# Optimization experiments

Measured on AMD Instinct MI355X. Metric: run time of the kernel, lower is better.

Reference implementation:

```python
import jax, jax.numpy as jnp
import numpy as np

N_NODES = 50000
N_EDGES = 400000
IN_DIM = 256
OUT_DIM = 64
HEADS = 2
ATTN_HIDDEN = 64
ALPHA = 0.2
TEMP = 0.55


def setup_inputs() -> dict:
    key = jax.random.key(0)
    k_x, k_src, k_dst, k_w, k_wa, k_a = jax.random.split(key, 6)
    x = jax.random.normal(k_x, (N_NODES, IN_DIM), dtype=jnp.float32)
    src = jax.random.randint(k_src, (N_EDGES,), 0, N_NODES, dtype=jnp.int32)
    dst = jnp.sort(jax.random.randint(k_dst, (N_EDGES,), 0, N_NODES, dtype=jnp.int32))
    # Glorot-uniform-like params
    def glorot(k, shape, fan_in, fan_out):
        lim = jnp.sqrt(6.0 / (fan_in + fan_out))
        return jax.random.uniform(k, shape, jnp.float32, -lim, lim)
    W = glorot(k_w, (IN_DIM, HEADS, OUT_DIM), IN_DIM, HEADS * OUT_DIM)
    W_attn = glorot(k_wa, (HEADS, 2 * OUT_DIM, ATTN_HIDDEN), 2 * OUT_DIM, ATTN_HIDDEN)
    a_vec = glorot(k_a, (HEADS, ATTN_HIDDEN), HEADS, ATTN_HIDDEN)
    return {"x": x, "W": W, "W_attn": W_attn, "a_vec": a_vec, "src": src, "dst": dst}


def reference(x, W, W_attn, a_vec, src, dst):
    N = x.shape[0]
    # node-level projection: [N, H, F]
    Wh = jnp.einsum('nd,dhf->nhf', x, W)
    # per-edge gathers
    Wh_src = Wh[src]                                   # [E, H, F]
    Wh_dst = Wh[dst]                                   # [E, H, F]
    z = jnp.concatenate([Wh_src, Wh_dst], axis=-1)     # [E, H, 2F]
    z_act = jax.nn.leaky_relu(jnp.einsum('ehf,hfc->ehc', z, W_attn), ALPHA)
    logits = jnp.einsum('ehc,hc->eh', z_act, a_vec).astype(jnp.float32) / TEMP
    # per-head segment softmax over incoming edges of each dst node
    seg_max = jax.ops.segment_max(logits, dst, num_segments=N)   # [N, H]
    ex = jnp.exp(logits - seg_max[dst])
    seg_sum = jax.ops.segment_sum(ex, dst, num_segments=N)
    alphas = (ex / (seg_sum[dst] + 1e-9)).astype(Wh_src.dtype)   # [E, H]
    # weighted scatter-sum of source messages
    out = jax.ops.segment_sum(Wh_src * alphas[..., None], dst, num_segments=N)  # [N, H, F]
    # concat=False -> mean over heads (dropout is identity at inference)
    return out.mean(axis=1)
```

## Files before the change

kernel.cpp:

```cpp
#include <hip/hip_runtime.h>
#include <hip/hip_bf16.h>
#include <math.h>

#define N_NODES 50000
#define N_EDGES 400000
#define IN_DIM 256
#define OUT_DIM 64
#define HEADS 2
#define ATTN_HIDDEN 64
#define ALPHA_SLOPE 0.2f
#define TEMP 0.55f
#define NHF 128
#define ZDIM 384

typedef __bf16 bf16x8 __attribute__((ext_vector_type(8)));
typedef float f32x4 __attribute__((ext_vector_type(4)));

__device__ __forceinline__ ushort f2bf(float f) {
    unsigned u = __float_as_uint(f);
    u = (u + 0x7fffu + ((u >> 16) & 1u)) >> 16;
    return (ushort)u;
}
__device__ __forceinline__ unsigned pack2(float a, float b) {
    return (unsigned)f2bf(a) | ((unsigned)f2bf(b) << 16);
}
__device__ __forceinline__ float bfl(unsigned u) { return __uint_as_float(u << 16); }
__device__ __forceinline__ float bfh(unsigned u) { return __uint_as_float(u & 0xffff0000u); }

__global__ __launch_bounds__(256) void k_combine(const float* __restrict__ W,
                                                 const float* __restrict__ Wa,
                                                 ushort* __restrict__ Wctf,
                                                 const int* __restrict__ dst,
                                                 int* __restrict__ seg) {
    __shared__ float col[64];
    const int b = blockIdx.x;
    const int t = threadIdx.x;
    if (b >= ZDIM) {
        int n = (b - ZDIM) * 256 + t;
        if (n > N_NODES) return;
        int lo = 0, hi = N_EDGES;
        while (lo < hi) {
            int mid = (lo + hi) >> 1;
            if (dst[mid] < n) lo = mid + 1; else hi = mid;
        }
        seg[n] = lo;
        return;
    }
    const int n = b;
    const int k = t;
    const int c = n >> 4, r16 = n & 15;
    const int kc = k >> 5, q = (k >> 3) & 3, j = k & 7;
    const size_t pos = (size_t)(((c * 8 + kc) * 64 + q * 16 + r16)) * 8 + j;

    float val;
    if (n < 128) {
        val = W[(size_t)k * NHF + n];
    } else {
        const int part = (n - 128) >> 7;
        const int idx = (n - 128) & 127;
        const int h = idx >> 6;
        const int cc = idx & 63;
        const int fb = part ? 64 : 0;
        if (t < 64) col[t] = Wa[(size_t)h * 8192 + (size_t)(fb + t) * 64 + cc];
        __syncthreads();
        const float* wr = W + (size_t)k * NHF + h * 64;
        float acc = 0.f;
#pragma unroll
        for (int f = 0; f < 64; f++) acc += wr[f] * col[f];
        val = acc;
    }
    Wctf[pos] = f2bf(val);
}

__global__ __launch_bounds__(256, 2) void k_gemm(const float* __restrict__ x,
                                                 const ushort* __restrict__ Wctf,
                                                 ushort* __restrict__ Zb) {
    __shared__ __align__(16) ushort Bs[32768];
    const int t = threadIdx.x;
    const int w = t >> 6, lane = t & 63;
    const int q = lane >> 4, r16 = lane & 15;
    const int cbase = blockIdx.x * 8;
    const int rowbase = blockIdx.y * 128 + w * 32;

    {
        const uint4* gs = (const uint4*)(Wctf + (size_t)blockIdx.x * 32768);
        uint4* ls = (uint4*)Bs;
#pragma unroll
        for (int i = 0; i < 16; i++) ls[i * 256 + t] = gs[i * 256 + t];
    }

    int rA0 = rowbase + r16;
    int rA1 = rowbase + 16 + r16;
    rA0 = rA0 < N_NODES ? rA0 : N_NODES - 1;
    rA1 = rA1 < N_NODES ? rA1 : N_NODES - 1;
    const float* xp0 = x + (size_t)rA0 * IN_DIM + q * 8;
    const float* xp1 = x + (size_t)rA1 * IN_DIM + q * 8;

    uint4 Areg[2][8];
#pragma unroll
    for (int kc = 0; kc < 8; kc++) {
        const float4 a00 = *(const float4*)(xp0 + kc * 32);
        const float4 a01 = *(const float4*)(xp0 + kc * 32 + 4);
        const float4 a10 = *(const float4*)(xp1 + kc * 32);
        const float4 a11 = *(const float4*)(xp1 + kc * 32 + 4);
        Areg[0][kc].x = pack2(a00.x, a00.y); Areg[0][kc].y = pack2(a00.z, a00.w);
        Areg[0][kc].z = pack2(a01.x, a01.y); Areg[0][kc].w = pack2(a01.z, a01.w);
        Areg[1][kc].x = pack2(a10.x, a10.y); Areg[1][kc].y = pack2(a10.z, a10.w);
        Areg[1][kc].z = pack2(a11.x, a11.y); Areg[1][kc].w = pack2(a11.z, a11.w);
    }

    f32x4 acc[2][8];
#pragma unroll
    for (int c = 0; c < 8; c++) {
        acc[0][c] = (f32x4){0.f, 0.f, 0.f, 0.f};
        acc[1][c] = (f32x4){0.f, 0.f, 0.f, 0.f};
    }

    __syncthreads();

#pragma unroll
    for (int kc = 0; kc < 8; kc++) {
        const bf16x8 af0 = *(const bf16x8*)&Areg[0][kc];
        const bf16x8 af1 = *(const bf16x8*)&Areg[1][kc];
#pragma unroll
        for (int c = 0; c < 8; c++) {
            const bf16x8 bf = *(const bf16x8*)&Bs[((c * 8 + kc) * 64 + lane) * 8];
            acc[0][c] = __builtin_amdgcn_mfma_f32_16x16x32_bf16(af0, bf, acc[0][c], 0, 0, 0);
            acc[1][c] = __builtin_amdgcn_mfma_f32_16x16x32_bf16(af1, bf, acc[1][c], 0, 0, 0);
        }
    }
#pragma unroll
    for (int mt = 0; mt < 2; mt++)
#pragma unroll
        for (int c = 0; c < 8; c++)
#pragma unroll
            for (int rr = 0; rr < 4; rr++) {
                const int row = rowbase + mt * 16 + q * 4 + rr;
                if (row < N_NODES)
                    Zb[(size_t)row * ZDIM + (cbase + c) * 16 + r16] = f2bf(acc[mt][c][rr]);
            }
}

__global__ __launch_bounds__(256) void k_fused(const ushort* __restrict__ Zb,
                                               const float* __restrict__ avec,
                                               const int* __restrict__ src,
                                               const int* __restrict__ seg,
                                               float* __restrict__ out) {
    const int lane = threadIdx.x & 63;
    const int wv = threadIdx.x >> 6;
    const int g = lane >> 4, l16 = lane & 15;
    const int n = blockIdx.x * 16 + wv * 4 + g;
    if (n >= N_NODES) return;
    const int choff = 8 * l16;

    const float4 af0 = *(const float4*)(avec + choff);
    const float4 af1 = *(const float4*)(avec + choff + 4);
    const float a[8] = {af0.x, af0.y, af0.z, af0.w, af1.x, af1.y, af1.z, af1.w};

    const uint4 udv = *(const uint4*)(Zb + (size_t)n * ZDIM + 256 + choff);
    const float ud[8] = {bfl(udv.x), bfh(udv.x), bfl(udv.y), bfh(udv.y),
                         bfl(udv.z), bfh(udv.z), bfl(udv.w), bfh(udv.w)};

    const int e0 = seg[n], e1 = seg[n + 1];
    float m = -INFINITY, l = 0.f;
    float acc[8] = {0.f, 0.f, 0.f, 0.f, 0.f, 0.f, 0.f, 0.f};

    uint4 us = make_uint4(0, 0, 0, 0), wh = us;
    if (e0 < e1) {
        const int s = src[e0];
        us = *(const uint4*)(Zb + (size_t)s * ZDIM + 128 + choff);
        wh = *(const uint4*)(Zb + (size_t)s * ZDIM + choff);
    }
    for (int e = e0; e < e1; e++) {
        const uint4 cus = us, cwh = wh;
        if (e + 1 < e1) {
            const int sn = src[e + 1];
            us = *(const uint4*)(Zb + (size_t)sn * ZDIM + 128 + choff);
            wh = *(const uint4*)(Zb + (size_t)sn * ZDIM + choff);
        }
        float p;
        {
            float v0, v1, s0, s1;
            v0 = bfl(cus.x) + ud[0]; v1 = bfh(cus.x) + ud[1];
            s0 = fmaxf(v0, ALPHA_SLOPE * v0); s1 = fmaxf(v1, ALPHA_SLOPE * v1);
            p = s0 * a[0] + s1 * a[1];
            v0 = bfl(cus.y) + ud[2]; v1 = bfh(cus.y) + ud[3];
            s0 = fmaxf(v0, ALPHA_SLOPE * v0); s1 = fmaxf(v1, ALPHA_SLOPE * v1);
            p += s0 * a[2] + s1 * a[3];
            v0 = bfl(cus.z) + ud[4]; v1 = bfh(cus.z) + ud[5];
            s0 = fmaxf(v0, ALPHA_SLOPE * v0); s1 = fmaxf(v1, ALPHA_SLOPE * v1);
            p += s0 * a[4] + s1 * a[5];
            v0 = bfl(cus.w) + ud[6]; v1 = bfh(cus.w) + ud[7];
            s0 = fmaxf(v0, ALPHA_SLOPE * v0); s1 = fmaxf(v1, ALPHA_SLOPE * v1);
            p += s0 * a[6] + s1 * a[7];
        }
        p += __shfl_xor(p, 1, 64);
        p += __shfl_xor(p, 2, 64);
        p += __shfl_xor(p, 4, 64);
        const float logit = p * (1.0f / TEMP);
        const float nm = fmaxf(m, logit);
        const float sc = __expf(m - nm);
        const float wgt = __expf(logit - nm);
        l = l * sc + wgt;
        acc[0] = acc[0] * sc + wgt * bfl(cwh.x);
        acc[1] = acc[1] * sc + wgt * bfh(cwh.x);
        acc[2] = acc[2] * sc + wgt * bfl(cwh.y);
        acc[3] = acc[3] * sc + wgt * bfh(cwh.y);
        acc[4] = acc[4] * sc + wgt * bfl(cwh.z);
        acc[5] = acc[5] * sc + wgt * bfh(cwh.z);
        acc[6] = acc[6] * sc + wgt * bfl(cwh.w);
        acc[7] = acc[7] * sc + wgt * bfh(cwh.w);
        m = nm;
    }
    const float inv = 0.5f / (l + 1e-9f);
#pragma unroll
    for (int j = 0; j < 8; j++) {
        const float v = acc[j] * inv;
        acc[j] = v + __shfl_xor(v, 8, 64);
    }
    if (l16 < 8) {
        float4 o0 = make_float4(acc[0], acc[1], acc[2], acc[3]);
        float4 o1 = make_float4(acc[4], acc[5], acc[6], acc[7]);
        float* op = out + (size_t)n * 64 + choff;
        *(float4*)op = o0;
        *(float4*)(op + 4) = o1;
    }
}

extern "C" void kernel_launch(void* const* d_in, const int* in_sizes, int n_in,
                              void* d_out, int out_size, void* d_ws, size_t ws_size,
                              hipStream_t stream) {
    const float* x    = (const float*)d_in[0];
    const float* W    = (const float*)d_in[1];
    const float* Wa   = (const float*)d_in[2];
    const float* avec = (const float*)d_in[3];
    const int*   src  = (const int*)d_in[4];
    const int*   dst  = (const int*)d_in[5];
    float* out = (float*)d_out;

    ushort* Zb   = (ushort*)d_ws;
    ushort* Wctf = Zb + 19200000;
    int*    seg  = (int*)((char*)d_ws + 38596608);

    const int seg_blocks = (N_NODES + 1 + 255) / 256;
    k_combine <<<ZDIM + seg_blocks, 256, 0, stream>>>(W, Wa, Wctf, dst, seg);
    k_gemm    <<<dim3(3, (N_NODES + 127) / 128), 256, 0, stream>>>(x, Wctf, Zb);
    k_fused   <<<(N_NODES + 15) / 16, 256, 0, stream>>>(Zb, avec, src, seg, out);
}
```

Before: 162.5 us.

## Restructure GEMM to load x once per block and loop over column tiles

The GEMM grid changes from 3 column blocks by row blocks of 128 to a single dimension of 64-row blocks. Each block now converts its x rows to bf16 once and loops over the three 128-column slices of the combined weight, reloading the weight slice into shared memory each time. Before, x was read from global memory three times, once per column block; now it is read once. The cost is three serial weight loads into LDS per block with extra barriers, smaller per-wave M tiles (16 rows instead of 32), and more blocks in total.

Measured after the change: 157.2 us. -3.3%, faster.

```diff
diff --git a/kernel.cpp b/kernel.cpp
--- a/kernel.cpp
+++ b/kernel.cpp
@@ -79,66 +79,64 @@
     const int t = threadIdx.x;
     const int w = t >> 6, lane = t & 63;
     const int q = lane >> 4, r16 = lane & 15;
-    const int cbase = blockIdx.x * 8;
-    const int rowbase = blockIdx.y * 128 + w * 32;
+    const int rowbase = blockIdx.x * 64 + w * 16;
 
     {
-        const uint4* gs = (const uint4*)(Wctf + (size_t)blockIdx.x * 32768);
+        const uint4* gs = (const uint4*)Wctf;
         uint4* ls = (uint4*)Bs;
 #pragma unroll
         for (int i = 0; i < 16; i++) ls[i * 256 + t] = gs[i * 256 + t];
     }
 
-    int rA0 = rowbase + r16;
-    int rA1 = rowbase + 16 + r16;
-    rA0 = rA0 < N_NODES ? rA0 : N_NODES - 1;
-    rA1 = rA1 < N_NODES ? rA1 : N_NODES - 1;
-    const float* xp0 = x + (size_t)rA0 * IN_DIM + q * 8;
-    const float* xp1 = x + (size_t)rA1 * IN_DIM + q * 8;
-
-    uint4 Areg[2][8];
+    int rA = rowbase + r16;
+    rA = rA < N_NODES ? rA : N_NODES - 1;
+    const float* xp = x + (size_t)rA * IN_DIM + q * 8;
+    uint4 Areg[8];
 #pragma unroll
     for (int kc = 0; kc < 8; kc++) {
-        const float4 a00 = *(const float4*)(xp0 + kc * 32);
-        const float4 a01 = *(const float4*)(xp0 + kc * 32 + 4);
-        const float4 a10 = *(const float4*)(xp1 + kc * 32);
-        const float4 a11 = *(const float4*)(xp1 + kc * 32 + 4);
-        Areg[0][kc].x = pack2(a00.x, a00.y); Areg[0][kc].y = pack2(a00.z, a00.w);
-        Areg[0][kc].z = pack2(a01.x, a01.y); Areg[0][kc].w = pack2(a01.z, a01.w);
-        Areg[1][kc].x = pack2(a10.x, a10.y); Areg[1][kc].y = pack2(a10.z, a10.w);
-        Areg[1][kc].z = pack2(a11.x, a11.y); Areg[1][kc].w = pack2(a11.z, a11.w);
-    }
-
-    f32x4 acc[2][8];
-#pragma unroll
-    for (int c = 0; c < 8; c++) {
-        acc[0][c] = (f32x4){0.f, 0.f, 0.f, 0.f};
-        acc[1][c] = (f32x4){0.f, 0.f, 0.f, 0.f};
+        const float4 a0 = *(const float4*)(xp + kc * 32);
+        const float4 a1 = *(const float4*)(xp + kc * 32 + 4);
+        Areg[kc].x = pack2(a0.x, a0.y); Areg[kc].y = pack2(a0.z, a0.w);
+        Areg[kc].z = pack2(a1.x, a1.y); Areg[kc].w = pack2(a1.z, a1.w);
     }
 
     __syncthreads();
 
-#pragma unroll
-    for (int kc = 0; kc < 8; kc++) {
-        const bf16x8 af0 = *(const bf16x8*)&Areg[0][kc];
-        const bf16x8 af1 = *(const bf16x8*)&Areg[1][kc];
-#pragma unroll
-        for (int c = 0; c < 8; c++) {
-            const bf16x8 bf = *(const bf16x8*)&Bs[((c * 8 + kc) * 64 + lane) * 8];
-            acc[0][c] = __builtin_amdgcn_mfma_f32_16x16x32_bf16(af0, bf, acc[0][c], 0, 0, 0);
-            acc[1][c] = __builtin_amdgcn_mfma_f32_16x16x32_bf16(af1, bf, acc[1][c], 0, 0, 0);
-        }
-    }
-#pragma unroll
-    for (int mt = 0; mt < 2; mt++)
+#pragma unroll 1
+    for (int s = 0; s < 3; s++) {
+        f32x4 acc[8];
+#pragma unroll
+        for (int c = 0; c < 8; c++) acc[c] = (f32x4){0.f, 0.f, 0.f, 0.f};
+
+#pragma unroll
+        for (int kc = 0; kc < 8; kc++) {
+            const bf16x8 af = *(const bf16x8*)&Areg[kc];
+#pragma unroll
+            for (int c = 0; c < 8; c++) {
+                const bf16x8 bf = *(const bf16x8*)&Bs[((c * 8 + kc) * 64 + lane) * 8];
+                acc[c] = __builtin_amdgcn_mfma_f32_16x16x32_bf16(af, bf, acc[c], 0, 0, 0);
+            }
+        }
+
+        if (s < 2) {
+            __syncthreads();
+            const uint4* gs = (const uint4*)Wctf + (size_t)(s + 1) * 4096;
+            uint4* ls = (uint4*)Bs;
+#pragma unroll
+            for (int i = 0; i < 16; i++) ls[i * 256 + t] = gs[i * 256 + t];
+        }
+
 #pragma unroll
         for (int c = 0; c < 8; c++)
 #pragma unroll
             for (int rr = 0; rr < 4; rr++) {
-                const int row = rowbase + mt * 16 + q * 4 + rr;
+                const int row = rowbase + q * 4 + rr;
                 if (row < N_NODES)
-                    Zb[(size_t)row * ZDIM + (cbase + c) * 16 + r16] = f2bf(acc[mt][c][rr]);
+                    Zb[(size_t)row * ZDIM + (s * 8 + c) * 16 + r16] = f2bf(acc[c][rr]);
             }
+
+        if (s < 2) __syncthreads();
+    }
 }
 
 __global__ __launch_bounds__(256) void k_fused(const ushort* __restrict__ Zb,
@@ -244,6 +242,6 @@
 
     const int seg_blocks = (N_NODES + 1 + 255) / 256;
     k_combine <<<ZDIM + seg_blocks, 256, 0, stream>>>(W, Wa, Wctf, dst, seg);
-    k_gemm    <<<dim3(3, (N_NODES + 127) / 128), 256, 0, stream>>>(x, Wctf, Zb);
+    k_gemm    <<<(N_NODES + 63) / 64, 256, 0, stream>>>(x, Wctf, Zb);
     k_fused   <<<(N_NODES + 15) / 16, 256, 0, stream>>>(Zb, avec, src, seg, out);
 }
```
